# Kernel tuning notes

Hardware: AMD Instinct MI355X
Metric: run time of the kernel (lower is better)

The kernel has to match this reference:

```python
import jax, jax.numpy as jnp
import numpy as np

N_HEADS = 12


def setup_inputs() -> dict:
    key = jax.random.key(0)
    k1, k2, k3 = jax.random.split(key, 3)
    B, W, C = 2, 2048, 768
    in_sequence_bwc = jax.random.normal(k1, (B, W, C), dtype=jnp.float32)
    # QKV projection weight [3C, C] (torch Linear convention: out_features x in_features)
    w_attn = jax.random.normal(k2, (3 * C, C), dtype=jnp.float32) * (1.0 / np.sqrt(C))
    w_proj = jax.random.normal(k3, (C, C), dtype=jnp.float32) * (1.0 / np.sqrt(C))
    return {"in_sequence_bwc": in_sequence_bwc, "w_attn": w_attn, "w_proj": w_proj}


def reference(in_sequence_bwc, w_attn, w_proj):
    B, W, C = in_sequence_bwc.shape
    H = N_HEADS
    K = C // H  # head dim
    qkv = jnp.einsum('bwc,dc->bwd', in_sequence_bwc, w_attn)  # [B,W,3C]
    q, k, v = jnp.split(qkv, 3, axis=-1)
    # [B,H,W,K]
    q = q.reshape(B, W, H, K).transpose(0, 2, 1, 3)
    k = k.reshape(B, W, H, K).transpose(0, 2, 1, 3)
    v = v.reshape(B, W, H, K).transpose(0, 2, 1, 3)
    scores = jnp.einsum('bhqk,bhsk->bhqs', q, k) / jnp.sqrt(jnp.float32(K))
    causal = jnp.tril(jnp.ones((W, W), dtype=bool))
    scores = jnp.where(causal[None, None], scores, jnp.float32(-jnp.inf))
    probs = jax.nn.softmax(scores, axis=-1)
    out = jnp.einsum('bhqs,bhsk->bhqk', probs, v)  # [B,H,W,K]
    out = out.transpose(0, 2, 1, 3).reshape(B, W, C)
    return jnp.einsum('bwc,dc->bwd', out, w_proj)
```

## Files before the change

### kernel.cpp

```cpp
#include <hip/hip_runtime.h>

constexpr int B_  = 2;
constexpr int W_  = 2048;
constexpr int C_  = 768;
constexpr int H_  = 12;
constexpr int HD  = 64;
constexpr int C3  = 3 * C_;
constexpr int M_  = B_ * W_;
constexpr int NSLOT = 80;

typedef float  f32x4 __attribute__((ext_vector_type(4)));
typedef short  s16x8 __attribute__((ext_vector_type(8)));
typedef short  s16x4 __attribute__((ext_vector_type(4)));
typedef unsigned short u16;
typedef unsigned int   u32;

__device__ __forceinline__ u16 f2bf(float f) {
    unsigned int u = __float_as_uint(f);
    u += 0x7FFFu + ((u >> 16) & 1u);
    return (u16)(u >> 16);
}

__device__ __forceinline__ void gload_lds16(const u16* g, u16* l) {
    __builtin_amdgcn_global_load_lds(
        (const __attribute__((address_space(1))) unsigned int*)g,
        (__attribute__((address_space(3))) unsigned int*)l, 16, 0, 0);
}

__global__ __launch_bounds__(256)
void cvt_all(const float* __restrict__ x, const float* __restrict__ wa,
             const float* __restrict__ wp, u16* __restrict__ xb,
             u16* __restrict__ wab, u16* __restrict__ wpb)
{
    const int n0 = M_ * C_ / 8;
    const int n1 = n0 + C3 * C_ / 8;
    const int n2 = n1 + C_ * C_ / 8;
    int i = blockIdx.x * 256 + threadIdx.x;
    const float* s; u16* d; int j;
    if (i < n0)      { s = x;  d = xb;  j = i; }
    else if (i < n1) { s = wa; d = wab; j = i - n0; }
    else if (i < n2) { s = wp; d = wpb; j = i - n1; }
    else return;
    const float4 a = reinterpret_cast<const float4*>(s)[j * 2];
    const float4 b = reinterpret_cast<const float4*>(s)[j * 2 + 1];
    s16x8 v;
    v[0] = (short)f2bf(a.x); v[1] = (short)f2bf(a.y);
    v[2] = (short)f2bf(a.z); v[3] = (short)f2bf(a.w);
    v[4] = (short)f2bf(b.x); v[5] = (short)f2bf(b.y);
    v[6] = (short)f2bf(b.z); v[7] = (short)f2bf(b.w);
    reinterpret_cast<s16x8*>(d)[j] = v;
}

__device__ __forceinline__ void store_out(u16*  p, float v) { *p = f2bf(v); }
__device__ __forceinline__ void store_out(float* p, float v) { *p = v; }

template <typename OutT>
__global__ __launch_bounds__(256)
void gemm_nt_mfma(const u16* __restrict__ A, const u16* __restrict__ Bm,
                  OutT* __restrict__ Y, int Ndim, int Kdim)
{
    __shared__ __align__(16) u16 As[2][128 * 64];
    __shared__ __align__(16) u16 Bs[2][128 * 64];

    const int t  = threadIdx.x;
    const int w  = t >> 6;
    const int l  = t & 63;
    const int lg = l >> 4;
    const int ln = l & 15;
    const int wm = w >> 1;
    const int wn = w & 1;
    const int m0 = blockIdx.x * 128;
    const int n0 = blockIdx.y * 128;

    f32x4 acc[4][4];
    #pragma unroll
    for (int mi = 0; mi < 4; ++mi)
        #pragma unroll
        for (int ni = 0; ni < 4; ++ni)
            acc[mi][ni] = (f32x4){0.f, 0.f, 0.f, 0.f};

    #define GEMM_STAGE(buf, k0s)                                              \
        _Pragma("unroll")                                                     \
        for (int it = 0; it < 4; ++it) {                                      \
            const int c  = t + it * 256;                                      \
            const int fr = c >> 7;                                            \
            const int s  = (c >> 6) & 1;                                      \
            const int kc = (c >> 4) & 3;                                      \
            const int rr = c & 15;                                            \
            const size_t koff = (size_t)(k0s) + s * 32 + kc * 8;              \
            gload_lds16(A  + (size_t)(m0 + fr * 16 + rr) * Kdim + koff,       \
                        &As[buf][(size_t)(it * 256 + w * 64) * 8]);           \
            gload_lds16(Bm + (size_t)(n0 + fr * 16 + rr) * Kdim + koff,       \
                        &Bs[buf][(size_t)(it * 256 + w * 64) * 8]);           \
        }

    GEMM_STAGE(0, 0)
    __syncthreads();

    int cur = 0;
    for (int k0 = 0; k0 < Kdim; k0 += 64) {
        if (k0 + 64 < Kdim) { GEMM_STAGE(cur ^ 1, k0 + 64) }

        #pragma unroll
        for (int s = 0; s < 2; ++s) {
            s16x8 af[4], bf[4];
            #pragma unroll
            for (int mi = 0; mi < 4; ++mi)
                af[mi] = *reinterpret_cast<const s16x8*>(
                    &As[cur][(size_t)((wm * 4 + mi) * 128 + s * 64 + lg * 16 + ln) * 8]);
            #pragma unroll
            for (int ni = 0; ni < 4; ++ni)
                bf[ni] = *reinterpret_cast<const s16x8*>(
                    &Bs[cur][(size_t)((wn * 4 + ni) * 128 + s * 64 + lg * 16 + ln) * 8]);
            __builtin_amdgcn_s_setprio(1);
            #pragma unroll
            for (int mi = 0; mi < 4; ++mi)
                #pragma unroll
                for (int ni = 0; ni < 4; ++ni)
                    acc[mi][ni] = __builtin_amdgcn_mfma_f32_16x16x32_bf16(
                        af[mi], bf[ni], acc[mi][ni], 0, 0, 0);
            __builtin_amdgcn_s_setprio(0);
        }

        __syncthreads();
        cur ^= 1;
    }
    #undef GEMM_STAGE

    #pragma unroll
    for (int mi = 0; mi < 4; ++mi) {
        const int row = m0 + wm * 64 + mi * 16 + lg * 4;
        #pragma unroll
        for (int ni = 0; ni < 4; ++ni) {
            const int col = n0 + wn * 64 + ni * 16 + ln;
            #pragma unroll
            for (int r = 0; r < 4; ++r)
                store_out(&Y[(size_t)(row + r) * Ndim + col], acc[mi][ni][r]);
        }
    }
}

__global__ __launch_bounds__(256)
void attn_partial(const u16* __restrict__ qkv, float* __restrict__ po,
                  float* __restrict__ pl)
{
    __shared__ __align__(16) unsigned char KsB[64 * 128];
    __shared__ __align__(16) unsigned char VtB[64 * 144];

    const int t  = threadIdx.x;
    const int w  = t >> 6;
    const int l  = t & 63;
    const int lg = l >> 4;
    const int ln = l & 15;
    const int p  = blockIdx.x;
    const int h  = blockIdx.y;
    const int b  = blockIdx.z;

    int qt, ck;
    if (p < 8)       { qt = p;                 ck = 0; }
    else if (p < 24) { qt = 8  + ((p - 8) >> 1);  ck = (p - 8) & 1; }
    else if (p < 48) { qt = 16 + (p - 24) / 3;    ck = (p - 24) % 3; }
    else             { qt = 24 + ((p - 48) >> 2); ck = (p - 48) & 3; }

    const int qb  = qt * 64;
    const int q0w = qb + w * 16;
    const int g0  = ck * 8;
    const int g1  = min(qt + 1, g0 + 8);
    const int slot = (b * H_ + h) * NSLOT + p;

    const u16* base  = qkv + (size_t)(b * W_) * C3;
    const u16* kbase = base + C_ + h * HD;
    const u16* vbase = base + 2 * C_ + h * HD;

    s16x8 qf[2];
    {
        const u16* qrow = base + (size_t)(q0w + ln) * C3 + h * HD;
        #pragma unroll
        for (int kc = 0; kc < 2; ++kc)
            qf[kc] = *reinterpret_cast<const s16x8*>(&qrow[kc * 32 + lg * 8]);
    }

    s16x8 onesf;
    {
        const short v1 = (ln == 0) ? (short)0x3F80 : (short)0;
        #pragma unroll
        for (int i = 0; i < 8; ++i) onesf[i] = v1;
    }

    f32x4 o[4];
    #pragma unroll
    for (int i = 0; i < 4; ++i) o[i] = (f32x4){0.f, 0.f, 0.f, 0.f};
    f32x4 o4 = (f32x4){0.f, 0.f, 0.f, 0.f};

    const float c1 = 0.18033688011112042f;
    const float c2 = 17.312340490667562f;

    const size_t sk_off = (size_t)((t >> 7) * 16 + (t & 15)) * C3
                        + ((t >> 6) & 1) * 32 + ((t >> 4) & 3) * 8;
    const bool vstage = (t < 128);
    const int vrun = (t >> 4) & 7;
    const int vK0  = (vrun >> 2) * 32 + (vrun & 3) * 4;
    const int vdq  = (t & 15) * 4;
    const int kfb  = l * 16;

    s16x8 kr[2];
    s16x4 vr[8];

    {
        const int s0 = g0 * 64;
        const u16* ks = kbase + (size_t)s0 * C3 + sk_off;
        kr[0] = *reinterpret_cast<const s16x8*>(ks);
        kr[1] = *reinterpret_cast<const s16x8*>(ks + (size_t)32 * C3);
        if (vstage) {
            const u16* vsrc = vbase + (size_t)(s0 + vK0) * C3 + vdq;
            #pragma unroll
            for (int e = 0; e < 8; ++e)
                vr[e] = *reinterpret_cast<const s16x4*>(
                    &vsrc[(size_t)((e >> 2) * 16 + (e & 3)) * C3]);
        }
    }

    for (int g = g0; g < g1; ++g) {
        const int s0 = g * 64;

        __syncthreads();

        *reinterpret_cast<s16x8*>(KsB + t * 16)         = kr[0];
        *reinterpret_cast<s16x8*>(KsB + (t + 256) * 16) = kr[1];
        if (vstage) {
            #pragma unroll
            for (int j = 0; j < 4; ++j) {
                s16x8 pk = { vr[0][j], vr[1][j], vr[2][j], vr[3][j],
                             vr[4][j], vr[5][j], vr[6][j], vr[7][j] };
                *reinterpret_cast<s16x8*>(
                    VtB + (vdq + j) * 144 + vrun * 16) = pk;
            }
        }

        if (g + 1 < g1) {
            const int s1 = s0 + 64;
            const u16* ks = kbase + (size_t)s1 * C3 + sk_off;
            kr[0] = *reinterpret_cast<const s16x8*>(ks);
            kr[1] = *reinterpret_cast<const s16x8*>(ks + (size_t)32 * C3);
            if (vstage) {
                const u16* vsrc = vbase + (size_t)(s1 + vK0) * C3 + vdq;
                #pragma unroll
                for (int e = 0; e < 8; ++e)
                    vr[e] = *reinterpret_cast<const s16x4*>(
                        &vsrc[(size_t)((e >> 2) * 16 + (e & 3)) * C3]);
            }
        }

        __syncthreads();

        #pragma unroll
        for (int c = 0; c < 2; ++c) {
            if (s0 + c * 32 <= q0w + 15) {
                float pt[2][4];
                #pragma unroll
                for (int n2 = 0; n2 < 2; ++n2) {
                    const unsigned char* kfrag = KsB + (c * 2 + n2) * 2048 + kfb;
                    s16x8 kf0 = *reinterpret_cast<const s16x8*>(kfrag);
                    s16x8 kf1 = *reinterpret_cast<const s16x8*>(kfrag + 1024);
                    f32x4 s = (f32x4){0.f, 0.f, 0.f, 0.f};
                    __builtin_amdgcn_s_setprio(1);
                    s = __builtin_amdgcn_mfma_f32_16x16x32_bf16(kf0, qf[0], s, 0, 0, 0);
                    s = __builtin_amdgcn_mfma_f32_16x16x32_bf16(kf1, qf[1], s, 0, 0, 0);
                    __builtin_amdgcn_s_setprio(0);
                    const int kg0   = s0 + c * 32 + n2 * 16 + lg * 4;
                    const int klast = s0 + c * 32 + n2 * 16 + 15;
                    if (klast <= q0w) {
                        #pragma unroll
                        for (int r = 0; r < 4; ++r)
                            pt[n2][r] = exp2f(fmaf(s[r], c1, -c2));
                    } else {
                        const int qg = q0w + ln;
                        #pragma unroll
                        for (int r = 0; r < 4; ++r)
                            pt[n2][r] = (kg0 + r <= qg)
                                      ? exp2f(fmaf(s[r], c1, -c2)) : 0.0f;
                    }
                }
                union { s16x8 v; u32 wd[4]; } afu;
                asm("v_cvt_pk_bf16_f32 %0, %1, %2"
                    : "=v"(afu.wd[0]) : "v"(pt[0][0]), "v"(pt[0][1]));
                asm("v_cvt_pk_bf16_f32 %0, %1, %2"
                    : "=v"(afu.wd[1]) : "v"(pt[0][2]), "v"(pt[0][3]));
                asm("v_cvt_pk_bf16_f32 %0, %1, %2"
                    : "=v"(afu.wd[2]) : "v"(pt[1][0]), "v"(pt[1][1]));
                asm("v_cvt_pk_bf16_f32 %0, %1, %2"
                    : "=v"(afu.wd[3]) : "v"(pt[1][2]), "v"(pt[1][3]));
                const s16x8 af = afu.v;
                s16x8 vf[4];
                #pragma unroll
                for (int dt = 0; dt < 4; ++dt)
                    vf[dt] = *reinterpret_cast<const s16x8*>(
                        VtB + (dt * 16 + ln) * 144 + c * 64 + lg * 16);
                __builtin_amdgcn_s_setprio(1);
                #pragma unroll
                for (int dt = 0; dt < 4; ++dt)
                    o[dt] = __builtin_amdgcn_mfma_f32_16x16x32_bf16(af, vf[dt], o[dt], 0, 0, 0);
                o4 = __builtin_amdgcn_mfma_f32_16x16x32_bf16(af, onesf, o4, 0, 0, 0);
                __builtin_amdgcn_s_setprio(0);
            }
        }
    }

    if (ln == 0) {
        #pragma unroll
        for (int r = 0; r < 4; ++r)
            pl[(size_t)slot * 64 + w * 16 + lg * 4 + r] = o4[r];
    }
    float* os = po + (size_t)slot * 4096;
    #pragma unroll
    for (int r = 0; r < 4; ++r)
        #pragma unroll
        for (int dt = 0; dt < 4; ++dt)
            os[(w * 16 + lg * 4 + r) * 64 + dt * 16 + ln] = o[dt][r];
}

__global__ __launch_bounds__(256)
void attn_combine(const float* __restrict__ po, const float* __restrict__ pl,
                  u16* __restrict__ aob)
{
    const int qt = blockIdx.x;
    const int h  = blockIdx.y;
    const int b  = blockIdx.z;
    const int nc = (qt + 8) >> 3;
    int cum;
    if (qt < 8)       cum = qt;
    else if (qt < 16) cum = 8  + 2 * (qt - 8);
    else if (qt < 24) cum = 24 + 3 * (qt - 16);
    else              cum = 48 + 4 * (qt - 24);
    const int slot0 = (b * H_ + h) * NSLOT + cum;

    const int tid = threadIdx.x;
    const int i   = tid >> 2;
    const int d0  = (tid & 3) * 16;

    f32x4 acc[4] = { (f32x4){0,0,0,0}, (f32x4){0,0,0,0},
                     (f32x4){0,0,0,0}, (f32x4){0,0,0,0} };
    float lt = 0.0f;
    for (int c = 0; c < nc; ++c) {
        const float* os = po + (size_t)(slot0 + c) * 4096 + i * 64 + d0;
        #pragma unroll
        for (int v = 0; v < 4; ++v)
            acc[v] += *reinterpret_cast<const f32x4*>(os + v * 4);
        lt += pl[(size_t)(slot0 + c) * 64 + i];
    }
    const float inv = 1.0f / lt;

    u16* dst = aob + (size_t)(b * W_ + qt * 64 + i) * C_ + h * HD + d0;
    s16x8 ov[2];
    #pragma unroll
    for (int v = 0; v < 4; ++v)
        #pragma unroll
        for (int e = 0; e < 4; ++e)
            ov[v >> 1][(v & 1) * 4 + e] = (short)f2bf(acc[v][e] * inv);
    *reinterpret_cast<s16x8*>(dst)     = ov[0];
    *reinterpret_cast<s16x8*>(dst + 8) = ov[1];
}

extern "C" void kernel_launch(void* const* d_in, const int* in_sizes, int n_in,
                              void* d_out, int out_size, void* d_ws, size_t ws_size,
                              hipStream_t stream)
{
    const float* x      = (const float*)d_in[0];
    const float* w_attn = (const float*)d_in[1];
    const float* w_proj = (const float*)d_in[2];
    float* out = (float*)d_out;

    u16* xb   = (u16*)d_ws;
    u16* wab  = xb   + (size_t)M_ * C_;
    u16* wpb  = wab  + (size_t)C3 * C_;
    u16* qkvb = wpb  + (size_t)C_ * C_;
    u16* aob  = qkvb + (size_t)M_ * C3;
    float* po = (float*)(aob + (size_t)M_ * C_);
    float* pl = po + (size_t)B_ * H_ * NSLOT * 4096;

    {
        const int total8 = (M_ * C_ + C3 * C_ + C_ * C_) / 8;
        cvt_all<<<(total8 + 255) / 256, 256, 0, stream>>>(
            x, w_attn, w_proj, xb, wab, wpb);
    }

    {
        dim3 grid(M_ / 128, C3 / 128);
        gemm_nt_mfma<u16><<<grid, 256, 0, stream>>>(xb, wab, qkvb, C3, C_);
    }

    {
        dim3 grid(NSLOT, H_, B_);
        attn_partial<<<grid, 256, 0, stream>>>(qkvb, po, pl);
    }
    {
        dim3 grid(W_ / 64, H_, B_);
        attn_combine<<<grid, 256, 0, stream>>>(po, pl, aob);
    }

    {
        dim3 grid(M_ / 128, C_ / 128);
        gemm_nt_mfma<float><<<grid, 256, 0, stream>>>(aob, wpb, out, C_, C_);
    }
}
```

Before: 126.2 us.

## Halve GEMM k-tile, store attention partials in bf16, reverse block order

The GEMM now stages 32-wide k-slices instead of 64, with precomputed load offsets and no setprio hints. This halves LDS use, which could allow more resident blocks, but doubles the number of barriers. Attention partial outputs are written as bf16 rather than fp32 to cut combine-stage memory traffic, at some accuracy cost. Partial blocks are also launched in reverse so the longest causal tiles start first.

```diff
diff --git a/kernel.cpp b/kernel.cpp
--- a/kernel.cpp
+++ b/kernel.cpp
@@ -19,6 +19,9 @@
     unsigned int u = __float_as_uint(f);
     u += 0x7FFFu + ((u >> 16) & 1u);
     return (u16)(u >> 16);
+}
+__device__ __forceinline__ float bf2f(u16 v) {
+    return __uint_as_float(((u32)v) << 16);
 }
 
 __device__ __forceinline__ void gload_lds16(const u16* g, u16* l) {
@@ -59,8 +62,8 @@
 void gemm_nt_mfma(const u16* __restrict__ A, const u16* __restrict__ Bm,
                   OutT* __restrict__ Y, int Ndim, int Kdim)
 {
-    __shared__ __align__(16) u16 As[2][128 * 64];
-    __shared__ __align__(16) u16 Bs[2][128 * 64];
+    __shared__ __align__(16) u16 As[2][128 * 32];
+    __shared__ __align__(16) u16 Bs[2][128 * 32];
 
     const int t  = threadIdx.x;
     const int w  = t >> 6;
@@ -79,18 +82,19 @@
         for (int ni = 0; ni < 4; ++ni)
             acc[mi][ni] = (f32x4){0.f, 0.f, 0.f, 0.f};
 
+    size_t off[2];
+    #pragma unroll
+    for (int it = 0; it < 2; ++it) {
+        const int c  = t + it * 256;
+        off[it] = (size_t)((c >> 6) * 16 + (c & 15)) * Kdim + ((c >> 4) & 3) * 8;
+    }
+
     #define GEMM_STAGE(buf, k0s)                                              \
         _Pragma("unroll")                                                     \
-        for (int it = 0; it < 4; ++it) {                                      \
-            const int c  = t + it * 256;                                      \
-            const int fr = c >> 7;                                            \
-            const int s  = (c >> 6) & 1;                                      \
-            const int kc = (c >> 4) & 3;                                      \
-            const int rr = c & 15;                                            \
-            const size_t koff = (size_t)(k0s) + s * 32 + kc * 8;              \
-            gload_lds16(A  + (size_t)(m0 + fr * 16 + rr) * Kdim + koff,       \
+        for (int it = 0; it < 2; ++it) {                                      \
+            gload_lds16(A  + (size_t)m0 * Kdim + (k0s) + off[it],             \
                         &As[buf][(size_t)(it * 256 + w * 64) * 8]);           \
-            gload_lds16(Bm + (size_t)(n0 + fr * 16 + rr) * Kdim + koff,       \
+            gload_lds16(Bm + (size_t)n0 * Kdim + (k0s) + off[it],             \
                         &Bs[buf][(size_t)(it * 256 + w * 64) * 8]);           \
         }
 
@@ -98,29 +102,24 @@
     __syncthreads();
 
     int cur = 0;
-    for (int k0 = 0; k0 < Kdim; k0 += 64) {
-        if (k0 + 64 < Kdim) { GEMM_STAGE(cur ^ 1, k0 + 64) }
-
-        #pragma unroll
-        for (int s = 0; s < 2; ++s) {
-            s16x8 af[4], bf[4];
-            #pragma unroll
-            for (int mi = 0; mi < 4; ++mi)
-                af[mi] = *reinterpret_cast<const s16x8*>(
-                    &As[cur][(size_t)((wm * 4 + mi) * 128 + s * 64 + lg * 16 + ln) * 8]);
+    for (int k0 = 0; k0 < Kdim; k0 += 32) {
+        if (k0 + 32 < Kdim) { GEMM_STAGE(cur ^ 1, k0 + 32) }
+
+        s16x8 af[4], bf[4];
+        #pragma unroll
+        for (int mi = 0; mi < 4; ++mi)
+            af[mi] = *reinterpret_cast<const s16x8*>(
+                &As[cur][(size_t)((wm * 4 + mi) * 64 + l) * 8]);
+        #pragma unroll
+        for (int ni = 0; ni < 4; ++ni)
+            bf[ni] = *reinterpret_cast<const s16x8*>(
+                &Bs[cur][(size_t)((wn * 4 + ni) * 64 + l) * 8]);
+        #pragma unroll
+        for (int mi = 0; mi < 4; ++mi)
             #pragma unroll
             for (int ni = 0; ni < 4; ++ni)
-                bf[ni] = *reinterpret_cast<const s16x8*>(
-                    &Bs[cur][(size_t)((wn * 4 + ni) * 128 + s * 64 + lg * 16 + ln) * 8]);
-            __builtin_amdgcn_s_setprio(1);
-            #pragma unroll
-            for (int mi = 0; mi < 4; ++mi)
-                #pragma unroll
-                for (int ni = 0; ni < 4; ++ni)
-                    acc[mi][ni] = __builtin_amdgcn_mfma_f32_16x16x32_bf16(
-                        af[mi], bf[ni], acc[mi][ni], 0, 0, 0);
-            __builtin_amdgcn_s_setprio(0);
-        }
+                acc[mi][ni] = __builtin_amdgcn_mfma_f32_16x16x32_bf16(
+                    af[mi], bf[ni], acc[mi][ni], 0, 0, 0);
 
         __syncthreads();
         cur ^= 1;
@@ -141,7 +140,7 @@
 }
 
 __global__ __launch_bounds__(256)
-void attn_partial(const u16* __restrict__ qkv, float* __restrict__ po,
+void attn_partial(const u16* __restrict__ qkv, u16* __restrict__ po,
                   float* __restrict__ pl)
 {
     __shared__ __align__(16) unsigned char KsB[64 * 128];
@@ -152,7 +151,7 @@
     const int l  = t & 63;
     const int lg = l >> 4;
     const int ln = l & 15;
-    const int p  = blockIdx.x;
+    const int p  = (NSLOT - 1) - (int)blockIdx.x;
     const int h  = blockIdx.y;
     const int b  = blockIdx.z;
 
@@ -311,16 +310,16 @@
         for (int r = 0; r < 4; ++r)
             pl[(size_t)slot * 64 + w * 16 + lg * 4 + r] = o4[r];
     }
-    float* os = po + (size_t)slot * 4096;
+    u16* os = po + (size_t)slot * 4096;
     #pragma unroll
     for (int r = 0; r < 4; ++r)
         #pragma unroll
         for (int dt = 0; dt < 4; ++dt)
-            os[(w * 16 + lg * 4 + r) * 64 + dt * 16 + ln] = o[dt][r];
+            os[(w * 16 + lg * 4 + r) * 64 + dt * 16 + ln] = f2bf(o[dt][r]);
 }
 
 __global__ __launch_bounds__(256)
-void attn_combine(const float* __restrict__ po, const float* __restrict__ pl,
+void attn_combine(const u16* __restrict__ po, const float* __restrict__ pl,
                   u16* __restrict__ aob)
 {
     const int qt = blockIdx.x;
@@ -338,14 +337,17 @@
     const int i   = tid >> 2;
     const int d0  = (tid & 3) * 16;
 
-    f32x4 acc[4] = { (f32x4){0,0,0,0}, (f32x4){0,0,0,0},
-                     (f32x4){0,0,0,0}, (f32x4){0,0,0,0} };
+    float acc[16] = {};
     float lt = 0.0f;
     for (int c = 0; c < nc; ++c) {
-        const float* os = po + (size_t)(slot0 + c) * 4096 + i * 64 + d0;
-        #pragma unroll
-        for (int v = 0; v < 4; ++v)
-            acc[v] += *reinterpret_cast<const f32x4*>(os + v * 4);
+        const u16* os = po + (size_t)(slot0 + c) * 4096 + i * 64 + d0;
+        s16x8 v0 = *reinterpret_cast<const s16x8*>(os);
+        s16x8 v1 = *reinterpret_cast<const s16x8*>(os + 8);
+        #pragma unroll
+        for (int e = 0; e < 8; ++e) {
+            acc[e]     += bf2f((u16)v0[e]);
+            acc[8 + e] += bf2f((u16)v1[e]);
+        }
         lt += pl[(size_t)(slot0 + c) * 64 + i];
     }
     const float inv = 1.0f / lt;
@@ -353,10 +355,10 @@
     u16* dst = aob + (size_t)(b * W_ + qt * 64 + i) * C_ + h * HD + d0;
     s16x8 ov[2];
     #pragma unroll
-    for (int v = 0; v < 4; ++v)
-        #pragma unroll
-        for (int e = 0; e < 4; ++e)
-            ov[v >> 1][(v & 1) * 4 + e] = (short)f2bf(acc[v][e] * inv);
+    for (int e = 0; e < 8; ++e) {
+        ov[0][e] = (short)f2bf(acc[e] * inv);
+        ov[1][e] = (short)f2bf(acc[8 + e] * inv);
+    }
     *reinterpret_cast<s16x8*>(dst)     = ov[0];
     *reinterpret_cast<s16x8*>(dst + 8) = ov[1];
 }
@@ -375,8 +377,8 @@
     u16* wpb  = wab  + (size_t)C3 * C_;
     u16* qkvb = wpb  + (size_t)C_ * C_;
     u16* aob  = qkvb + (size_t)M_ * C3;
-    float* po = (float*)(aob + (size_t)M_ * C_);
-    float* pl = po + (size_t)B_ * H_ * NSLOT * 4096;
+    u16* po   = aob  + (size_t)M_ * C_;
+    float* pl = (float*)(po + (size_t)B_ * H_ * NSLOT * 4096);
 
     {
         const int total8 = (M_ * C_ + C3 * C_ + C_ * C_) / 8;
```

After: 118.3 us. 6.3% less time.
